# Performance work log

Measured on AMD Instinct MI355X. Metric: run time of the kernel, lower is better.

## Reference

```python
import jax, jax.numpy as jnp
import numpy as np

WIN = 8
NUM_LAYERS = 2
HID = 512
GROUPS = 4
GH = 2 * HID // GROUPS  # 256


def _shuffle(y):
    # torch Shuffle: transpose(-1,-2).contiguous().view(original_shape)
    return jnp.swapaxes(y, -1, -2).reshape(y.shape)


def _gru_cell(xt, h, w_ih, w_hh, b_ih, b_hh):
    # torch.nn.GRUCell math; gate order r, z, n
    gi = xt @ w_ih.T + b_ih  # [B, 3H]
    gh = h @ w_hh.T + b_hh   # [B, 3H]
    i_r, i_z, i_n = jnp.split(gi, 3, axis=1)
    h_r, h_z, h_n = jnp.split(gh, 3, axis=1)
    r = jax.nn.sigmoid(i_r + h_r)
    z = jax.nn.sigmoid(i_z + h_z)
    n = jnp.tanh(i_n + r * h_n)
    return (1.0 - z) * n + z * h


def _sort_attn(h, a1, a2, a3, a4):
    B, H = h.shape
    s = jnp.sort(h, axis=1)                 # stable sort along features
    se = jnp.stack((h, s), axis=1)          # [B, 2, H]
    y = se @ a1.T                           # Linear(H, H) -> [B, 2, H]
    y = y.reshape(B, GROUPS, GH)            # Flatten + Unflatten
    y = _shuffle(y)
    y = y @ a2.T                            # Linear(GH, GH)
    y = _shuffle(y)
    y = jax.nn.relu(y @ a3.T)               # Linear(GH, GH) + ReLU
    y = y.reshape(B, GROUPS * GH)           # [B, 2H]
    scores = jax.nn.sigmoid(y @ a4.T)       # Linear(2H, H) -> [B, H]
    return h * scores


def setup_inputs() -> dict:
    key = jax.random.key(0)
    ks = jax.random.split(key, 10)
    B, L, C = 64, 4096, 64
    sc = 0.05
    inp = {
        "x": jax.random.normal(ks[0], (B, L, C), dtype=jnp.float32),
        "hidden0": jnp.zeros((NUM_LAYERS, 1, HID), dtype=jnp.float32),
        "w_ih": jax.random.normal(ks[1], (NUM_LAYERS, 3 * HID, HID), dtype=jnp.float32) * sc,
        "w_hh": jax.random.normal(ks[2], (NUM_LAYERS, 3 * HID, HID), dtype=jnp.float32) * sc,
        "b_ih": jax.random.normal(ks[3], (NUM_LAYERS, 3 * HID), dtype=jnp.float32) * sc,
        "b_hh": jax.random.normal(ks[4], (NUM_LAYERS, 3 * HID), dtype=jnp.float32) * sc,
        "a1": jax.random.normal(ks[5], (NUM_LAYERS, HID, HID), dtype=jnp.float32) * sc,
        "a2": jax.random.normal(ks[6], (NUM_LAYERS, GH, GH), dtype=jnp.float32) * sc,
        "a3": jax.random.normal(ks[7], (NUM_LAYERS, GH, GH), dtype=jnp.float32) * sc,
        "a4": jax.random.normal(ks[8], (NUM_LAYERS, HID, 2 * HID), dtype=jnp.float32) * sc,
    }
    return inp


def reference(x, hidden0, w_ih, w_hh, b_ih, b_hh, a1, a2, a3, a4):
    B, L, C = x.shape
    xp = x.reshape(B, L // WIN, WIN * C)
    xs = jnp.swapaxes(xp, 0, 1)                       # [T, B, D]
    h0 = jnp.broadcast_to(hidden0, (NUM_LAYERS, B, HID))

    def step(hid, xt):
        inp = xt
        new = []
        for l in range(NUM_LAYERS):
            h = _gru_cell(inp, hid[l], w_ih[l], w_hh[l], b_ih[l], b_hh[l])
            h = _sort_attn(h, a1[l], a2[l], a3[l], a4[l])
            new.append(h)
            inp = h
        return jnp.stack(new, axis=0), inp

    _, outs = jax.lax.scan(step, h0, xs)              # outs: [T, B, H]
    return jnp.swapaxes(outs, 0, 1)                   # [B, T, H]
```

## Files before the change

### kernel.cpp

```cpp
#include <hip/hip_runtime.h>

#define SCOPE_AGENT __HIP_MEMORY_SCOPE_AGENT

#define OFF_HS    0
#define OFF_HP    65536
#define OFF_SG    131072
#define OFF_U     196608
#define OFF_CTR   327680
#define OFF_T1    393216
#define OFF_M     2490368
#define OFF_GIX   4587520
#define OFF_XT    4587520
#define WS_GIX    54919168
#define WS_XT     21364736

typedef float f32x4 __attribute__((ext_vector_type(4)));

__device__ __forceinline__ float sigm(float x) { return 1.f / (1.f + expf(-x)); }

__device__ __forceinline__ float ld_sc1(const float* p) {
    return __hip_atomic_load(p, __ATOMIC_RELAXED, SCOPE_AGENT);
}
__device__ __forceinline__ void st_sc1(float* p, float v) {
    __hip_atomic_store(p, v, __ATOMIC_RELAXED, SCOPE_AGENT);
}
__device__ __forceinline__ void st2(float* p, float a, float b) {
    unsigned long long v = ((unsigned long long)__float_as_uint(b) << 32) |
                           (unsigned long long)__float_as_uint(a);
    __hip_atomic_store((unsigned long long*)p, v, __ATOMIC_RELAXED, SCOPE_AGENT);
}

__device__ __forceinline__ void ld4b8(const float* base, f32x4* v) {
    const float* b2 = base + 1024;
    asm volatile(
        "global_load_dwordx4 %0, %8, off sc1\n\t"
        "global_load_dwordx4 %1, %8, off offset:1024 sc1\n\t"
        "global_load_dwordx4 %2, %8, off offset:2048 sc1\n\t"
        "global_load_dwordx4 %3, %8, off offset:3072 sc1\n\t"
        "global_load_dwordx4 %4, %9, off sc1\n\t"
        "global_load_dwordx4 %5, %9, off offset:1024 sc1\n\t"
        "global_load_dwordx4 %6, %9, off offset:2048 sc1\n\t"
        "global_load_dwordx4 %7, %9, off offset:3072 sc1\n\t"
        "s_waitcnt vmcnt(0)"
        : "=&v"(v[0]), "=&v"(v[1]), "=&v"(v[2]), "=&v"(v[3]),
          "=&v"(v[4]), "=&v"(v[5]), "=&v"(v[6]), "=&v"(v[7])
        : "v"(base), "v"(b2)
        : "memory");
}

__device__ __forceinline__ void gbar(unsigned* flags, unsigned* genr, unsigned g) {
    __syncthreads();
    const int tid = threadIdx.x;
    if (blockIdx.x == 0) {
        if (tid >= 1 && tid < 256) {
            while (__hip_atomic_load(&flags[tid << 5], __ATOMIC_RELAXED, SCOPE_AGENT) < g)
                __builtin_amdgcn_s_sleep(1);
        }
        __syncthreads();
        if (tid < 16)
            __hip_atomic_store(&genr[tid << 5], g, __ATOMIC_RELAXED, SCOPE_AGENT);
        __syncthreads();
    } else {
        if (tid == 0) {
            __hip_atomic_store(&flags[blockIdx.x << 5], g, __ATOMIC_RELAXED, SCOPE_AGENT);
            while (__hip_atomic_load(&genr[(blockIdx.x & 15) << 5], __ATOMIC_RELAXED, SCOPE_AGENT) < g)
                __builtin_amdgcn_s_sleep(1);
        }
        __syncthreads();
    }
}

__global__ void k_init(const float* __restrict__ h0, float* __restrict__ ws) {
    int idx = blockIdx.x * blockDim.x + threadIdx.x;
    int l = idx >> 15, k = (idx & 32767) >> 6, lane = idx & 63;
    ws[OFF_HS + (l << 15) + ((k >> 2) << 8) + (lane << 2) + (k & 3)] = h0[(l << 9) + k];
    if (idx < 8704) ((unsigned*)(ws + OFF_CTR))[idx] = 0u;
}

__global__ void k_gix(const float* __restrict__ x, const float* __restrict__ wih,
                      float* __restrict__ gix) {
    __shared__ float xs[128][65];
    __shared__ float ww[32][129];
    int t = blockIdx.x, rb = blockIdx.y * 32;
    int tid = threadIdx.x;
    int rw = tid >> 6, b = tid & 63;
    float acc[8] = {0.f, 0.f, 0.f, 0.f, 0.f, 0.f, 0.f, 0.f};
    for (int kc = 0; kc < 4; kc++) {
        __syncthreads();
        for (int i = tid; i < 8192; i += 256) {
            int k = i & 127, b2 = i >> 7;
            xs[k][b2] = x[(size_t)b2 * 262144 + (size_t)t * 512 + kc * 128 + k];
        }
        for (int i = tid; i < 4096; i += 256) {
            int r = i >> 7, k = i & 127;
            ww[r][k] = wih[(size_t)(rb + r) * 512 + kc * 128 + k];
        }
        __syncthreads();
        for (int k = 0; k < 128; k++) {
            float xv = xs[k][b];
#pragma unroll
            for (int rr = 0; rr < 8; rr++)
                acc[rr] = fmaf(ww[rw * 8 + rr][k], xv, acc[rr]);
        }
    }
#pragma unroll
    for (int rr = 0; rr < 8; rr++) {
        int rg = rb + rw * 8 + rr;
        int g = rg >> 9, j = rg & 511;
        gix[((size_t)((size_t)t * 512 + j) * 3 + g) * 64 + b] = acc[rr];
    }
}

__global__ void k_xtk(const float* __restrict__ x, float* __restrict__ xT) {
    __shared__ float tile[64][65];
    int t = blockIdx.x >> 3, kc = blockIdx.x & 7;
    int k = threadIdx.x & 63, b0 = threadIdx.x >> 6;
    for (int i = 0; i < 16; i++) {
        int b = i * 4 + b0;
        tile[k][b] = x[(size_t)b * 262144 + (size_t)t * 512 + kc * 64 + k];
    }
    __syncthreads();
    int b2 = threadIdx.x & 63, k0 = threadIdx.x >> 6;
    for (int i = 0; i < 16; i++) {
        int k2 = kc * 64 + i * 4 + k0;
        xT[(size_t)t * 32768 + ((k2 >> 2) << 8) + (b2 << 2) + (k2 & 3)] = tile[i * 4 + k0][b2];
    }
}

__global__ void k_t1(const float* __restrict__ a1, const float* __restrict__ a2,
                     float* __restrict__ T1) {
    int l = blockIdx.x >> 10, c = blockIdx.x & 1023;
    int g = c >> 8, jj = c & 255;
    __shared__ float sA2[256];
    sA2[threadIdx.x] = a2[l * 65536 + jj * 256 + threadIdx.x];
    __syncthreads();
    const float* A1l = a1 + l * 262144;
    for (int colq = 0; colq < 4; colq++) {
        int col = colq * 256 + threadIdx.x;
        int half = col >> 9, cm = col & 511;
        float acc = 0.f;
#pragma unroll 4
        for (int q = 0; q < 64; q++) {
            int a0 = 2 * half;
            int j0 = g * 64 + q;
            acc = fmaf(sA2[4 * q + a0],     A1l[j0 * 512 + cm], acc);
            acc = fmaf(sA2[4 * q + a0 + 1], A1l[(j0 + 256) * 512 + cm], acc);
        }
        T1[((size_t)(l << 10) + c) * 1024 + col] = acc;
    }
}

__global__ void k_m(const float* __restrict__ a3, const float* __restrict__ T1,
                    float* __restrict__ M) {
    int l = blockIdx.x >> 10, c = blockIdx.x & 1023;
    int g = c >> 8, jj = c & 255;
    __shared__ float sA3[256];
    sA3[threadIdx.x] = a3[l * 65536 + jj * 256 + threadIdx.x];
    __syncthreads();
    const float* T1l = T1 + ((size_t)l << 20);
    for (int colq = 0; colq < 4; colq++) {
        int col = colq * 256 + threadIdx.x;
        float acc = 0.f;
#pragma unroll 4
        for (int m = 0; m < 256; m++) {
            int p = ((m & 3) << 8) + (g << 6) + (m >> 2);
            acc = fmaf(sA3[m], T1l[p * 1024 + col], acc);
        }
        M[((size_t)(l << 10) + c) * 1024 + col] = acc;
    }
}

__global__ void __launch_bounds__(1024, 4)
persist(const float* __restrict__ x, const float* __restrict__ xT,
        const float* __restrict__ gix, int has_xt, int has_gix,
        const float* __restrict__ wih, const float* __restrict__ whh,
        const float* __restrict__ bih, const float* __restrict__ bhh,
        const float* __restrict__ Mc, const float* __restrict__ a4,
        float* __restrict__ ws, float* __restrict__ out) {
    __shared__ float wA[2][2][6][512];
    __shared__ float wM[2][4][1024];
    __shared__ float wD[2][2][1024];
    __shared__ float red2[12][16][64];
    __shared__ float bb[2][2][4];
    __shared__ float sH[2][2][64];

    const int tid = threadIdx.x, w = tid >> 6, lane = tid & 63, bid = blockIdx.x;

    for (int i = tid; i < 12288; i += 1024) {
        int l = i / 6144, r = i % 6144, f = r / 3072, r2 = r % 3072, d = r2 / 512, k = r2 & 511;
        int gate = d >> 1, side = d & 1;
        int j = 2 * bid + f;
        const float* src = side ? whh : wih;
        wA[l][f][d][k] = src[l * 786432 + (gate * 512 + j) * 512 + k];
    }
    for (int i = tid; i < 8192; i += 1024) {
        int l = i >> 12, r = (i >> 10) & 3, col = i & 1023;
        wM[l][r][col] = Mc[((size_t)(l << 10) + 4 * bid + r) * 1024 + col];
    }
    for (int i = tid; i < 4096; i += 1024) {
        int l = i >> 11, f = (i >> 10) & 1, k = i & 1023;
        wD[l][f][k] = a4[l * 524288 + (2 * bid + f) * 1024 + k];
    }
    if (tid < 16) {
        int l = tid / 8, f = (tid / 4) & 1, g = tid & 3;
        int j = 2 * bid + f;
        float v;
        if (g == 0)      v = bih[l * 1536 + j] + bhh[l * 1536 + j];
        else if (g == 1) v = bih[l * 1536 + 512 + j] + bhh[l * 1536 + 512 + j];
        else if (g == 2) v = bih[l * 1536 + 1024 + j];
        else             v = bhh[l * 1536 + 1024 + j];
        bb[l][f][g] = v;
    }
    __syncthreads();

    float* hsG = ws + OFF_HS;
    float* hPg = ws + OFF_HP;
    float* sGg = ws + OFF_SG;
    float* uG  = ws + OFF_U;
    unsigned* flags = (unsigned*)(ws + OFF_CTR);
    unsigned* genr  = flags + 8192;
    unsigned bgen = 0;

    auto stageA = [&](int l, int t) {
        float hprev = 0.f;
        if (w < 2) {
            int j = 2 * bid + w;
            hprev = ld_sc1(&hsG[(l << 15) + ((j >> 2) << 8) + (lane << 2) + (j & 3)]);
        }
        const float* hb = hsG + (l << 15);
        float* hPl = hPg + (l << 15);
        int k0 = w * 32;
        if (l == 0 && has_gix) {
            float acc[6] = {0.f, 0.f, 0.f, 0.f, 0.f, 0.f};
            f32x4 hv[8];
            ld4b8(hb + ((k0 >> 2) << 8) + (lane << 2), hv);
#pragma unroll
            for (int m = 0; m < 8; m++) {
#pragma unroll
                for (int q = 0; q < 4; q++) {
                    int k = k0 + 4 * m + q;
                    float h = hv[m][q];
#pragma unroll
                    for (int f = 0; f < 2; f++) {
                        acc[f * 3 + 0] = fmaf(wA[0][f][1][k], h, acc[f * 3 + 0]);
                        acc[f * 3 + 1] = fmaf(wA[0][f][3][k], h, acc[f * 3 + 1]);
                        acc[f * 3 + 2] = fmaf(wA[0][f][5][k], h, acc[f * 3 + 2]);
                    }
                }
            }
#pragma unroll
            for (int u = 0; u < 6; u++) red2[u][w][lane] = acc[u];
            __syncthreads();
            if (w < 2) {
                int f = w, j = 2 * bid + f;
                float s0 = 0, s1 = 0, s2 = 0;
#pragma unroll
                for (int i = 0; i < 16; i++) {
                    s0 += red2[f * 3 + 0][i][lane];
                    s1 += red2[f * 3 + 1][i][lane];
                    s2 += red2[f * 3 + 2][i][lane];
                }
                const float* gx = gix + ((size_t)((size_t)t * 512 + j) * 3) * 64;
                float r = sigm(gx[lane] + s0 + bb[0][f][0]);
                float z = sigm(gx[64 + lane] + s1 + bb[0][f][1]);
                float n = tanhf(gx[128 + lane] + bb[0][f][2] + r * (s2 + bb[0][f][3]));
                float hp = (1.f - z) * n + z * hprev;
                sH[0][f][lane] = hp;
                st_sc1(&hPl[((j >> 2) << 8) + (lane << 2) + (j & 3)], hp);
            }
        } else {
            float acc[12];
#pragma unroll
            for (int u = 0; u < 12; u++) acc[u] = 0.f;
            {
                f32x4 iv[8];
                if (l == 1) {
                    ld4b8(hsG + ((k0 >> 2) << 8) + (lane << 2), iv);
                } else if (has_xt) {
                    ld4b8(xT + (size_t)t * 32768 + ((k0 >> 2) << 8) + (lane << 2), iv);
                } else {
#pragma unroll
                    for (int m = 0; m < 8; m++)
#pragma unroll
                        for (int q = 0; q < 4; q++)
                            iv[m][q] = x[(size_t)lane * 262144 + (size_t)t * 512 + k0 + 4 * m + q];
                }
#pragma unroll
                for (int m = 0; m < 8; m++) {
#pragma unroll
                    for (int q = 0; q < 4; q++) {
                        int k = k0 + 4 * m + q;
                        float ivq = iv[m][q];
#pragma unroll
                        for (int f = 0; f < 2; f++) {
                            acc[f * 6 + 0] = fmaf(wA[l][f][0][k], ivq, acc[f * 6 + 0]);
                            acc[f * 6 + 2] = fmaf(wA[l][f][2][k], ivq, acc[f * 6 + 2]);
                            acc[f * 6 + 4] = fmaf(wA[l][f][4][k], ivq, acc[f * 6 + 4]);
                        }
                    }
                }
            }
            {
                f32x4 hv[8];
                ld4b8(hb + ((k0 >> 2) << 8) + (lane << 2), hv);
#pragma unroll
                for (int m = 0; m < 8; m++) {
#pragma unroll
                    for (int q = 0; q < 4; q++) {
                        int k = k0 + 4 * m + q;
                        float h = hv[m][q];
#pragma unroll
                        for (int f = 0; f < 2; f++) {
                            acc[f * 6 + 1] = fmaf(wA[l][f][1][k], h, acc[f * 6 + 1]);
                            acc[f * 6 + 3] = fmaf(wA[l][f][3][k], h, acc[f * 6 + 3]);
                            acc[f * 6 + 5] = fmaf(wA[l][f][5][k], h, acc[f * 6 + 5]);
                        }
                    }
                }
            }
#pragma unroll
            for (int u = 0; u < 12; u++) red2[u][w][lane] = acc[u];
            __syncthreads();
            if (w < 2) {
                int f = w, j = 2 * bid + f;
                float g0 = 0, g1 = 0, g2 = 0, g3 = 0, g4 = 0, g5 = 0;
#pragma unroll
                for (int i = 0; i < 16; i++) {
                    g0 += red2[f * 6 + 0][i][lane]; g1 += red2[f * 6 + 1][i][lane];
                    g2 += red2[f * 6 + 2][i][lane]; g3 += red2[f * 6 + 3][i][lane];
                    g4 += red2[f * 6 + 4][i][lane]; g5 += red2[f * 6 + 5][i][lane];
                }
                float r = sigm(g0 + g1 + bb[l][f][0]);
                float z = sigm(g2 + g3 + bb[l][f][1]);
                float n = tanhf(g4 + bb[l][f][2] + r * (g5 + bb[l][f][3]));
                float hp = (1.f - z) * n + z * hprev;
                sH[l][f][lane] = hp;
                st_sc1(&hPl[((j >> 2) << 8) + (lane << 2) + (j & 3)], hp);
            }
        }
    };

    auto stageB = [&](int l, float* accB) {
        int j0 = 2 * bid, j1 = j0 + 1;
        float v0 = sH[l][0][lane], v1 = sH[l][1][lane];
        const float* hPl = hPg + (l << 15);
        float* sGl = sGg + (l << 15);
        int k0 = w * 32, cnt0 = 0, cnt1 = 0;
        accB[0] = accB[1] = accB[2] = accB[3] = 0.f;
        f32x4 hv[8];
        ld4b8(hPl + ((k0 >> 2) << 8) + (lane << 2), hv);
#pragma unroll
        for (int m = 0; m < 8; m++) {
#pragma unroll
            for (int q = 0; q < 4; q++) {
                int k = k0 + 4 * m + q;
                float h = hv[m][q];
                cnt0 += (h < v0 || (h == v0 && k < j0)) ? 1 : 0;
                cnt1 += (h < v1 || (h == v1 && k < j1)) ? 1 : 0;
#pragma unroll
                for (int r = 0; r < 4; r++)
                    accB[r] = fmaf(wM[l][r][k], h, accB[r]);
            }
        }
        red2[0][w][lane] = (float)cnt0;
        red2[1][w][lane] = (float)cnt1;
        __syncthreads();
        if (w < 2) {
            int rk = 0;
#pragma unroll
            for (int i = 0; i < 16; i++) rk += (int)red2[w][i][lane];
            st_sc1(&sGl[((rk >> 2) << 8) + (lane << 2) + (rk & 3)], sH[l][w][lane]);
        }
    };

    auto stageC = [&](int l, const float* accB) {
        float acc[4] = {accB[0], accB[1], accB[2], accB[3]};
        int s0 = w * 32;
        const float* sGl = sGg + (l << 15);
        f32x4 sv[8];
        ld4b8(sGl + ((s0 >> 2) << 8) + (lane << 2), sv);
#pragma unroll
        for (int m = 0; m < 8; m++) {
#pragma unroll
            for (int q = 0; q < 4; q++) {
                int sp = s0 + 4 * m + q;
                float vv = sv[m][q];
#pragma unroll
                for (int r = 0; r < 4; r++)
                    acc[r] = fmaf(wM[l][r][512 + sp], vv, acc[r]);
            }
        }
#pragma unroll
        for (int r = 0; r < 4; r++) red2[r][w][lane] = acc[r];
        __syncthreads();
        if (w < 2) {
            float sa = 0.f, sb = 0.f;
#pragma unroll
            for (int i = 0; i < 16; i++) {
                sa += red2[2 * w + 0][i][lane];
                sb += red2[2 * w + 1][i][lane];
            }
            st2(&uG[(l << 16) + (bid << 8) + (lane << 2) + (w << 1)],
                fmaxf(sa, 0.f), fmaxf(sb, 0.f));
        }
    };

    auto stageD = [&](int l, int t) {
        float a0 = 0.f, a1v = 0.f;
        int k0 = w * 64;
        const float* uL = uG + (l << 16);
        {
            f32x4 uv[8];
            ld4b8(uL + ((k0 >> 2) << 8) + (lane << 2), uv);
#pragma unroll
            for (int m = 0; m < 8; m++)
#pragma unroll
                for (int q = 0; q < 4; q++) {
                    int k = k0 + 4 * m + q;
                    a0 = fmaf(wD[l][0][k], uv[m][q], a0);
                    a1v = fmaf(wD[l][1][k], uv[m][q], a1v);
                }
        }
        {
            f32x4 uv[8];
            ld4b8(uL + (((k0 >> 2) + 8) << 8) + (lane << 2), uv);
#pragma unroll
            for (int m = 0; m < 8; m++)
#pragma unroll
                for (int q = 0; q < 4; q++) {
                    int k = k0 + 32 + 4 * m + q;
                    a0 = fmaf(wD[l][0][k], uv[m][q], a0);
                    a1v = fmaf(wD[l][1][k], uv[m][q], a1v);
                }
        }
        red2[0][w][lane] = a0;
        red2[1][w][lane] = a1v;
        __syncthreads();
        if (w < 2) {
            float s = 0.f;
#pragma unroll
            for (int i = 0; i < 16; i++) s += red2[w][i][lane];
            float hnew = sH[l][w][lane] * sigm(s);
            int j = 2 * bid + w;
            st_sc1(&hsG[(l << 15) + ((j >> 2) << 8) + (lane << 2) + (j & 3)], hnew);
            if (l == 1)
                out[(size_t)lane * 262144 + (size_t)t * 512 + j] = hnew;
        }
    };

    float accB0[4], accB1[4];

    for (int t = 0; t <= 512; t++) {
        const int t0 = t, t1 = t - 1;
        const bool do0 = (t0 < 512), do1 = (t1 >= 0);

        if (do0) stageA(0, t0);
        if (do1) { __syncthreads(); stageA(1, t1); }
        gbar(flags, genr, ++bgen);

        if (do0) stageB(0, accB0);
        if (do1) { __syncthreads(); stageB(1, accB1); }
        gbar(flags, genr, ++bgen);

        if (do0) stageC(0, accB0);
        if (do1) { __syncthreads(); stageC(1, accB1); }
        gbar(flags, genr, ++bgen);

        if (do0) stageD(0, t0);
        if (do1) { __syncthreads(); stageD(1, t1); }
        gbar(flags, genr, ++bgen);
    }
}

extern "C" void kernel_launch(void* const* d_in, const int* in_sizes, int n_in,
                              void* d_out, int out_size, void* d_ws, size_t ws_size,
                              hipStream_t stream) {
    const float* x   = (const float*)d_in[0];
    const float* h0  = (const float*)d_in[1];
    const float* wih = (const float*)d_in[2];
    const float* whh = (const float*)d_in[3];
    const float* bih = (const float*)d_in[4];
    const float* bhh = (const float*)d_in[5];
    const float* a1  = (const float*)d_in[6];
    const float* a2  = (const float*)d_in[7];
    const float* a3  = (const float*)d_in[8];
    const float* a4  = (const float*)d_in[9];
    float* ws  = (float*)d_ws;
    float* out = (float*)d_out;

    int has_gix = (ws_size >= (size_t)WS_GIX * 4) ? 1 : 0;
    int has_xt  = (!has_gix && ws_size >= (size_t)WS_XT * 4) ? 1 : 0;
    float* T1p = ws + OFF_T1;
    float* Mp  = ws + OFF_M;
    const float* gixp = ws + OFF_GIX;
    const float* xTp  = ws + OFF_XT;

    hipLaunchKernelGGL(k_init, dim3(256), dim3(256), 0, stream, h0, ws);
    if (has_gix)
        hipLaunchKernelGGL(k_gix, dim3(512, 48), dim3(256), 0, stream, x, wih, ws + OFF_GIX);
    else if (has_xt)
        hipLaunchKernelGGL(k_xtk, dim3(4096), dim3(256), 0, stream, x, ws + OFF_XT);
    hipLaunchKernelGGL(k_t1, dim3(2048), dim3(256), 0, stream, a1, a2, T1p);
    hipLaunchKernelGGL(k_m, dim3(2048), dim3(256), 0, stream, a3, T1p, Mp);

    void* args[] = {(void*)&x, (void*)&xTp, (void*)&gixp, (void*)&has_xt, (void*)&has_gix,
                    (void*)&wih, (void*)&whh, (void*)&bih, (void*)&bhh,
                    (void*)&Mp, (void*)&a4, (void*)&ws, (void*)&out};
    hipLaunchCooperativeKernel((void*)persist, dim3(256), dim3(1024), args, 0, stream);
}
```

Before: 43.96 ms.

## Replace two-level grid barrier with all-to-all flag polling and batch global loads

The grid barrier no longer goes through block 0 gathering flags and broadcasting a release generation. Every block now publishes its own flag, and each block's first 256 threads poll all 256 flags directly, which cuts one round-trip of latency per barrier. Separately, the input and hidden-state vector loads in stageA and the two u loads in stageD are issued together in one asm block with a single waitcnt, so their memory latencies overlap. The costs are more polling traffic on the flag lines and higher register pressure from holding 16 vectors at once.

```diff
diff --git a/kernel.cpp b/kernel.cpp
--- a/kernel.cpp
+++ b/kernel.cpp
@@ -48,26 +48,46 @@
         : "memory");
 }
 
-__device__ __forceinline__ void gbar(unsigned* flags, unsigned* genr, unsigned g) {
+__device__ __forceinline__ void ld4b8x2(const float* baseA, const float* baseB,
+                                        f32x4* va, f32x4* vb) {
+    const float* a2 = baseA + 1024;
+    const float* b2 = baseB + 1024;
+    asm volatile(
+        "global_load_dwordx4 %0, %16, off sc1\n\t"
+        "global_load_dwordx4 %1, %16, off offset:1024 sc1\n\t"
+        "global_load_dwordx4 %2, %16, off offset:2048 sc1\n\t"
+        "global_load_dwordx4 %3, %16, off offset:3072 sc1\n\t"
+        "global_load_dwordx4 %4, %17, off sc1\n\t"
+        "global_load_dwordx4 %5, %17, off offset:1024 sc1\n\t"
+        "global_load_dwordx4 %6, %17, off offset:2048 sc1\n\t"
+        "global_load_dwordx4 %7, %17, off offset:3072 sc1\n\t"
+        "global_load_dwordx4 %8, %18, off sc1\n\t"
+        "global_load_dwordx4 %9, %18, off offset:1024 sc1\n\t"
+        "global_load_dwordx4 %10, %18, off offset:2048 sc1\n\t"
+        "global_load_dwordx4 %11, %18, off offset:3072 sc1\n\t"
+        "global_load_dwordx4 %12, %19, off sc1\n\t"
+        "global_load_dwordx4 %13, %19, off offset:1024 sc1\n\t"
+        "global_load_dwordx4 %14, %19, off offset:2048 sc1\n\t"
+        "global_load_dwordx4 %15, %19, off offset:3072 sc1\n\t"
+        "s_waitcnt vmcnt(0)"
+        : "=&v"(va[0]), "=&v"(va[1]), "=&v"(va[2]), "=&v"(va[3]),
+          "=&v"(va[4]), "=&v"(va[5]), "=&v"(va[6]), "=&v"(va[7]),
+          "=&v"(vb[0]), "=&v"(vb[1]), "=&v"(vb[2]), "=&v"(vb[3]),
+          "=&v"(vb[4]), "=&v"(vb[5]), "=&v"(vb[6]), "=&v"(vb[7])
+        : "v"(baseA), "v"(a2), "v"(baseB), "v"(b2)
+        : "memory");
+}
+
+__device__ __forceinline__ void gbar(unsigned* flags, unsigned g) {
     __syncthreads();
     const int tid = threadIdx.x;
-    if (blockIdx.x == 0) {
-        if (tid >= 1 && tid < 256) {
-            while (__hip_atomic_load(&flags[tid << 5], __ATOMIC_RELAXED, SCOPE_AGENT) < g)
-                __builtin_amdgcn_s_sleep(1);
-        }
-        __syncthreads();
-        if (tid < 16)
-            __hip_atomic_store(&genr[tid << 5], g, __ATOMIC_RELAXED, SCOPE_AGENT);
-        __syncthreads();
-    } else {
-        if (tid == 0) {
-            __hip_atomic_store(&flags[blockIdx.x << 5], g, __ATOMIC_RELAXED, SCOPE_AGENT);
-            while (__hip_atomic_load(&genr[(blockIdx.x & 15) << 5], __ATOMIC_RELAXED, SCOPE_AGENT) < g)
-                __builtin_amdgcn_s_sleep(1);
-        }
-        __syncthreads();
-    }
+    if (tid == 0)
+        __hip_atomic_store(&flags[blockIdx.x << 5], g, __ATOMIC_RELAXED, SCOPE_AGENT);
+    if (tid < 256) {
+        while (__hip_atomic_load(&flags[tid << 5], __ATOMIC_RELAXED, SCOPE_AGENT) < g)
+            __builtin_amdgcn_s_sleep(1);
+    }
+    __syncthreads();
 }
 
 __global__ void k_init(const float* __restrict__ h0, float* __restrict__ ws) {
@@ -218,7 +238,6 @@
     float* sGg = ws + OFF_SG;
     float* uG  = ws + OFF_U;
     unsigned* flags = (unsigned*)(ws + OFF_CTR);
-    unsigned* genr  = flags + 8192;
     unsigned bgen = 0;
 
     auto stageA = [&](int l, int t) {
@@ -230,10 +249,11 @@
         const float* hb = hsG + (l << 15);
         float* hPl = hPg + (l << 15);
         int k0 = w * 32;
+        const int koff = ((k0 >> 2) << 8) + (lane << 2);
         if (l == 0 && has_gix) {
             float acc[6] = {0.f, 0.f, 0.f, 0.f, 0.f, 0.f};
             f32x4 hv[8];
-            ld4b8(hb + ((k0 >> 2) << 8) + (lane << 2), hv);
+            ld4b8(hb + koff, hv);
 #pragma unroll
             for (int m = 0; m < 8; m++) {
 #pragma unroll
@@ -272,49 +292,44 @@
             float acc[12];
 #pragma unroll
             for (int u = 0; u < 12; u++) acc[u] = 0.f;
-            {
-                f32x4 iv[8];
-                if (l == 1) {
-                    ld4b8(hsG + ((k0 >> 2) << 8) + (lane << 2), iv);
-                } else if (has_xt) {
-                    ld4b8(xT + (size_t)t * 32768 + ((k0 >> 2) << 8) + (lane << 2), iv);
-                } else {
-#pragma unroll
-                    for (int m = 0; m < 8; m++)
-#pragma unroll
-                        for (int q = 0; q < 4; q++)
-                            iv[m][q] = x[(size_t)lane * 262144 + (size_t)t * 512 + k0 + 4 * m + q];
-                }
-#pragma unroll
-                for (int m = 0; m < 8; m++) {
-#pragma unroll
-                    for (int q = 0; q < 4; q++) {
-                        int k = k0 + 4 * m + q;
-                        float ivq = iv[m][q];
-#pragma unroll
-                        for (int f = 0; f < 2; f++) {
-                            acc[f * 6 + 0] = fmaf(wA[l][f][0][k], ivq, acc[f * 6 + 0]);
-                            acc[f * 6 + 2] = fmaf(wA[l][f][2][k], ivq, acc[f * 6 + 2]);
-                            acc[f * 6 + 4] = fmaf(wA[l][f][4][k], ivq, acc[f * 6 + 4]);
-                        }
+            f32x4 iv[8], hv[8];
+            if (l == 1) {
+                ld4b8x2(hsG + koff, hb + koff, iv, hv);
+            } else if (has_xt) {
+                ld4b8x2(xT + (size_t)t * 32768 + koff, hb + koff, iv, hv);
+            } else {
+#pragma unroll
+                for (int m = 0; m < 8; m++)
+#pragma unroll
+                    for (int q = 0; q < 4; q++)
+                        iv[m][q] = x[(size_t)lane * 262144 + (size_t)t * 512 + k0 + 4 * m + q];
+                ld4b8(hb + koff, hv);
+            }
+#pragma unroll
+            for (int m = 0; m < 8; m++) {
+#pragma unroll
+                for (int q = 0; q < 4; q++) {
+                    int k = k0 + 4 * m + q;
+                    float ivq = iv[m][q];
+#pragma unroll
+                    for (int f = 0; f < 2; f++) {
+                        acc[f * 6 + 0] = fmaf(wA[l][f][0][k], ivq, acc[f * 6 + 0]);
+                        acc[f * 6 + 2] = fmaf(wA[l][f][2][k], ivq, acc[f * 6 + 2]);
+                        acc[f * 6 + 4] = fmaf(wA[l][f][4][k], ivq, acc[f * 6 + 4]);
                     }
                 }
             }
-            {
-                f32x4 hv[8];
-                ld4b8(hb + ((k0 >> 2) << 8) + (lane << 2), hv);
-#pragma unroll
-                for (int m = 0; m < 8; m++) {
-#pragma unroll
-                    for (int q = 0; q < 4; q++) {
-                        int k = k0 + 4 * m + q;
-                        float h = hv[m][q];
-#pragma unroll
-                        for (int f = 0; f < 2; f++) {
-                            acc[f * 6 + 1] = fmaf(wA[l][f][1][k], h, acc[f * 6 + 1]);
-                            acc[f * 6 + 3] = fmaf(wA[l][f][3][k], h, acc[f * 6 + 3]);
-                            acc[f * 6 + 5] = fmaf(wA[l][f][5][k], h, acc[f * 6 + 5]);
-                        }
+#pragma unroll
+            for (int m = 0; m < 8; m++) {
+#pragma unroll
+                for (int q = 0; q < 4; q++) {
+                    int k = k0 + 4 * m + q;
+                    float h = hv[m][q];
+#pragma unroll
+                    for (int f = 0; f < 2; f++) {
+                        acc[f * 6 + 1] = fmaf(wA[l][f][1][k], h, acc[f * 6 + 1]);
+                        acc[f * 6 + 3] = fmaf(wA[l][f][3][k], h, acc[f * 6 + 3]);
+                        acc[f * 6 + 5] = fmaf(wA[l][f][5][k], h, acc[f * 6 + 5]);
                     }
                 }
             }
@@ -409,30 +424,25 @@
         float a0 = 0.f, a1v = 0.f;
         int k0 = w * 64;
         const float* uL = uG + (l << 16);
-        {
-            f32x4 uv[8];
-            ld4b8(uL + ((k0 >> 2) << 8) + (lane << 2), uv);
-#pragma unroll
-            for (int m = 0; m < 8; m++)
-#pragma unroll
-                for (int q = 0; q < 4; q++) {
-                    int k = k0 + 4 * m + q;
-                    a0 = fmaf(wD[l][0][k], uv[m][q], a0);
-                    a1v = fmaf(wD[l][1][k], uv[m][q], a1v);
-                }
-        }
-        {
-            f32x4 uv[8];
-            ld4b8(uL + (((k0 >> 2) + 8) << 8) + (lane << 2), uv);
-#pragma unroll
-            for (int m = 0; m < 8; m++)
-#pragma unroll
-                for (int q = 0; q < 4; q++) {
-                    int k = k0 + 32 + 4 * m + q;
-                    a0 = fmaf(wD[l][0][k], uv[m][q], a0);
-                    a1v = fmaf(wD[l][1][k], uv[m][q], a1v);
-                }
-        }
+        f32x4 uv[8], uw[8];
+        ld4b8x2(uL + ((k0 >> 2) << 8) + (lane << 2),
+                uL + (((k0 >> 2) + 8) << 8) + (lane << 2), uv, uw);
+#pragma unroll
+        for (int m = 0; m < 8; m++)
+#pragma unroll
+            for (int q = 0; q < 4; q++) {
+                int k = k0 + 4 * m + q;
+                a0 = fmaf(wD[l][0][k], uv[m][q], a0);
+                a1v = fmaf(wD[l][1][k], uv[m][q], a1v);
+            }
+#pragma unroll
+        for (int m = 0; m < 8; m++)
+#pragma unroll
+            for (int q = 0; q < 4; q++) {
+                int k = k0 + 32 + 4 * m + q;
+                a0 = fmaf(wD[l][0][k], uw[m][q], a0);
+                a1v = fmaf(wD[l][1][k], uw[m][q], a1v);
+            }
         red2[0][w][lane] = a0;
         red2[1][w][lane] = a1v;
         __syncthreads();
@@ -456,19 +466,19 @@
 
         if (do0) stageA(0, t0);
         if (do1) { __syncthreads(); stageA(1, t1); }
-        gbar(flags, genr, ++bgen);
+        gbar(flags, ++bgen);
 
         if (do0) stageB(0, accB0);
         if (do1) { __syncthreads(); stageB(1, accB1); }
-        gbar(flags, genr, ++bgen);
+        gbar(flags, ++bgen);
 
         if (do0) stageC(0, accB0);
         if (do1) { __syncthreads(); stageC(1, accB1); }
-        gbar(flags, genr, ++bgen);
+        gbar(flags, ++bgen);
 
         if (do0) stageD(0, t0);
         if (do1) { __syncthreads(); stageD(1, t1); }
-        gbar(flags, genr, ++bgen);
+        gbar(flags, ++bgen);
     }
 }
 
```

Result: no change. 43.46 ms, median of 2 (-1.1%).
